# Performance work log

Hardware: AMD Instinct MI355X
Metric: run time of the kernel (lower is better)

## Reference

```python
import jax, jax.numpy as jnp
import numpy as np

# Module hyperparameters (match torch init_kwargs)
D_MODEL = 512
N_HEADS = 8
WINDOW_LEN = 128
DIL_FACTOR = 64
N_DIL = 2
ATTN_SINK = True
SRC_LEN = 2048
BSZ = 2


def setup_inputs() -> dict:
    key = jax.random.key(0)
    ks = jax.random.split(key, 6)
    w_scale = 0.04  # ~ xavier_uniform scale for 512x512
    inp = {
        "x": jax.random.normal(ks[0], (SRC_LEN, BSZ, D_MODEL), jnp.float32),
        "Wq": jax.random.normal(ks[1], (D_MODEL, D_MODEL), jnp.float32) * w_scale,
        "bq": jnp.zeros((D_MODEL,), jnp.float32),
        "Wk": jax.random.normal(ks[2], (D_MODEL, D_MODEL), jnp.float32) * w_scale,
        "bk": jnp.zeros((D_MODEL,), jnp.float32),
        "Wv": jax.random.normal(ks[3], (D_MODEL, D_MODEL), jnp.float32) * w_scale,
        "bv": jnp.zeros((D_MODEL,), jnp.float32),
        "Wo": jax.random.normal(ks[4], (D_MODEL, D_MODEL), jnp.float32) * w_scale,
        "bo": jnp.zeros((D_MODEL,), jnp.float32),
        "beta": jnp.zeros((N_HEADS,), jnp.float32),
    }
    return inp


def _fast_attention(x, Wq, bq, Wk, bk, Wv, bv, Wo, bo, beta):
    s, b, dm = x.shape  # (src_len, bsz, d_model)
    h = N_HEADS
    d = dm // h
    q = x @ Wq.T + bq
    k = x @ Wk.T + bk
    v = x @ Wv.T + bv

    def split_heads(t):  # 's b (h d) -> (b h) s d'
        return t.reshape(s, b, h, d).transpose(1, 2, 0, 3).reshape(b * h, s, d)

    q, k, v = split_heads(q), split_heads(k), split_heads(v)

    # beta: per-head temperature, tiled over batch (matches torch .repeat(bsz,1,1))
    beta_e = jnp.tile(jnp.exp(beta), b)[:, None, None]  # (b*h, 1, 1)
    q = q / (jnp.sqrt(jnp.asarray(d, q.dtype)) * beta_e)

    attn_out = jnp.zeros_like(v)
    z = b * h
    for i in range(N_DIL):
        dil = DIL_FACTOR ** i
        p = (WINDOW_LEN - 1) * dil
        pad = (p % s) if (p % s) != p else 0  # static python ints
        nw = pad // dil + 1  # num windows
        # causal left-padded strided windowed view of q: (z, nw, s, d)
        qp = jnp.pad(q, ((0, 0), (pad, 0), (0, 0)))
        idx = (jnp.arange(nw) * dil)[:, None] + jnp.arange(s)[None, :]  # (nw, s)
        qi = qp[:, idx, :]
        w = jnp.einsum('zbsd,zsd->zbs', qi, k)  # (z, nw, s)
        if ATTN_SINK:
            w = jnp.concatenate([w, jnp.zeros((z, 1, s), w.dtype)], axis=1)
        w = jax.nn.softmax(w, axis=1)  # softmax over window axis (+ sink)
        if ATTN_SINK:
            w = w[:, :-1]
        k2 = jnp.einsum('zbs,zsd->zbd', w, k)  # (z, nw, d)
        v2 = jnp.einsum('zbs,zsd->zbd', w, v)
        # left-pad back to full length (zeros at front, values at end)
        k = jnp.pad(k2, ((0, 0), (s - nw, 0), (0, 0)))
        v = jnp.pad(v2, ((0, 0), (s - nw, 0), (0, 0)))
        attn_out = attn_out + v

    # '(b h) s d -> s b (h d)'
    out = attn_out.reshape(b, h, s, d).transpose(2, 0, 1, 3).reshape(s, b, dm)
    return out @ Wo.T + bo


def reference(x, Wq, bq, Wk, bk, Wv, bv, Wo, bo, beta):
    return _fast_attention(x, Wq, bq, Wk, bk, Wv, bv, Wo, bo, beta)
```

## Files before the change

kernel.cpp:

```cpp
#include <hip/hip_runtime.h>
#include <hip/hip_bf16.h>
#include <math.h>

#define S_LEN 2048
#define BSZ 2
#define DM 512
#define NH 8
#define HD 64
#define RTOT (S_LEN*BSZ)
#define T_KEEP 32
#define ROW0 ((S_LEN - T_KEEP)*BSZ)
#define NXELEM (RTOT*DM)
#define NWROW  (NH*128)
#define NWELEM (NWROW*DM)

typedef __attribute__((ext_vector_type(8))) _Float16 half8;
typedef __attribute__((ext_vector_type(4))) float floatx4;

__device__ __forceinline__ void gld16(const void* g, void* l) {
    __builtin_amdgcn_global_load_lds((const __attribute__((address_space(1))) void*)g,
                                     (__attribute__((address_space(3))) void*)l, 16, 0, 0);
}

__device__ __forceinline__ short cvt1(float v) {
    _Float16 h = (_Float16)v;
    return __builtin_bit_cast(short, h);
}

__global__ __launch_bounds__(256) void convert(
    const float* __restrict__ x,
    const float* __restrict__ Wq, const float* __restrict__ Wk,
    const float* __restrict__ bq, const float* __restrict__ bk,
    const float* __restrict__ bo,
    short* __restrict__ xf, short* __restrict__ wf, float* __restrict__ bcat,
    float* __restrict__ sig, float* __restrict__ sbar, float* __restrict__ Ssum,
    float* __restrict__ out)
{
    const int g = blockIdx.x*blockDim.x + threadIdx.x;
    const int stride = gridDim.x*blockDim.x;
    const int total4 = (NXELEM + NWELEM)/4;
    for (int i = g; i < total4; i += stride) {
        float4 v; size_t dst; short* d;
        if (i < NXELEM/4) {
            v = ((const float4*)x)[i];
            dst = (size_t)i*4; d = xf;
        } else {
            int e = (i - NXELEM/4)*4;
            int R = e >> 9;
            int k = e & 511;
            int h = R >> 7;
            int p = R & 127;
            int m = p >> 6;
            int c = p & 63;
            const float* W = m ? Wk : Wq;
            v = *(const float4*)&W[(size_t)(h*HD + c)*DM + k];
            dst = (size_t)R*DM + k; d = wf;
        }
        short4 hv;
        hv.x = cvt1(v.x); hv.y = cvt1(v.y); hv.z = cvt1(v.z); hv.w = cvt1(v.w);
        *(short4*)&d[dst] = hv;
    }
    {
        const float4* b4 = (const float4*)bo;
        float4* o4 = (float4*)out;
        const int fill4 = ROW0*DM/4;
        for (int i = g; i < fill4; i += stride) o4[i] = b4[i & 127];
    }
    if (g < NWROW) {
        int h = g >> 7, p = g & 127, m = p >> 6, c = p & 63;
        bcat[g] = (m ? bk : bq)[h*HD + c];
    }
    if (g < NH*RTOT) sig[g] = 0.f;
    if (g < 16*DM)   sbar[g] = 0.f;
    if (g < 16)      Ssum[g] = 0.f;
}

__global__ __launch_bounds__(256, 2) void qk_gemm(
    const _Float16* __restrict__ xf, const _Float16* __restrict__ wf,
    const float* __restrict__ bcat,
    float* __restrict__ sig, float* __restrict__ qsel)
{
    __shared__ __align__(16) char smem[65536];

    const int tid  = threadIdx.x;
    const int w    = tid >> 6;
    const int lane = tid & 63;
    const int lrow = lane & 15;
    const int lk8  = lane >> 4;
    const int rc   = blockIdx.x;
    const int h    = blockIdx.y;
    const int jh   = blockIdx.z;
    const int r0   = rc * 128;

    {
        const int t = w;
        const int bcol = (t < 2) ? (jh*32 + t*16) : (64 + jh*32 + (t-2)*16);
        const _Float16* src = wf + (size_t)(h*128 + bcol + lrow)*DM + lk8*8;
        for (int ci = 0; ci < 16; ++ci)
            gld16(src + ci*32, smem + (w*16 + ci)*1024);
    }
    __syncthreads();

    const float bq0 = bcat[h*128 + jh*32 + lrow];
    const float bq1 = bcat[h*128 + jh*32 + 16 + lrow];
    const float bk0 = bcat[h*128 + 64 + jh*32 + lrow];
    const float bk1 = bcat[h*128 + 64 + jh*32 + 16 + lrow];

    #pragma unroll
    for (int nn = 0; nn < 2; ++nn) {
        const int n = w + nn*4;
        const int rbase = r0 + n*16;

        half8 A[16];
        const _Float16* pa = xf + (size_t)(rbase + lrow)*DM + lk8*8;
        #pragma unroll
        for (int kc = 0; kc < 16; ++kc)
            A[kc] = *(const half8*)(pa + kc*32);

        floatx4 aq0 = (floatx4)0.f, aq1 = (floatx4)0.f;
        floatx4 ak0 = (floatx4)0.f, ak1 = (floatx4)0.f;
        #pragma unroll
        for (int kc = 0; kc < 16; ++kc) {
            half8 b0 = *(const half8*)(smem + ( 0 + kc)*1024 + lane*16);
            half8 b1 = *(const half8*)(smem + (16 + kc)*1024 + lane*16);
            half8 b2 = *(const half8*)(smem + (32 + kc)*1024 + lane*16);
            half8 b3 = *(const half8*)(smem + (48 + kc)*1024 + lane*16);
            aq0 = __builtin_amdgcn_mfma_f32_16x16x32_f16(A[kc], b0, aq0, 0, 0, 0);
            aq1 = __builtin_amdgcn_mfma_f32_16x16x32_f16(A[kc], b1, aq1, 0, 0, 0);
            ak0 = __builtin_amdgcn_mfma_f32_16x16x32_f16(A[kc], b2, ak0, 0, 0, 0);
            ak1 = __builtin_amdgcn_mfma_f32_16x16x32_f16(A[kc], b3, ak1, 0, 0, 0);
        }

        #pragma unroll
        for (int r = 0; r < 4; ++r) {
            float q0 = aq0[r] + bq0, q1 = aq1[r] + bq1;
            float k0 = ak0[r] + bk0, k1 = ak1[r] + bk1;
            float p = q0*k0 + q1*k1;
            p += __shfl_xor(p, 1, 64);
            p += __shfl_xor(p, 2, 64);
            p += __shfl_xor(p, 4, 64);
            p += __shfl_xor(p, 8, 64);
            int row = rbase + lk8*4 + r;
            if (lrow == 0) atomicAdd(&sig[h*RTOT + row], p);
            if (((row >> 1) & 63) == 63) {
                int b  = row & 1;
                int wi = row >> 7;
                float* qd = &qsel[((size_t)(b*NH + h)*T_KEEP + wi)*64];
                qd[jh*32 + lrow]      = q0;
                qd[jh*32 + 16 + lrow] = q1;
            }
        }
    }
}

__global__ __launch_bounds__(256) void sbark(
    const float* __restrict__ x, const float* __restrict__ sigr,
    const float* __restrict__ beta, float* __restrict__ sbar,
    float* __restrict__ Ssum)
{
    __shared__ float ss[64][NH];
    const int tid = threadIdx.x;
    const int b = blockIdx.x & 1;
    const int s0 = (blockIdx.x >> 1) * 64;

    for (int i = tid; i < 64*NH; i += 256) {
        int s = i >> 3, hh = i & 7;
        float raw = sigr[hh*RTOT + (s0 + s)*2 + b];
        float isc = 1.0f / (8.0f * expf(beta[hh]));
        ss[s][hh] = 1.0f / (1.0f + expf(-raw * isc));
    }
    __syncthreads();
    if (tid < NH) {
        float t = 0.f;
        for (int s = 0; s < 64; ++s) t += ss[s][tid];
        atomicAdd(&Ssum[b*NH + tid], t);
    }
    #pragma unroll
    for (int cp = 0; cp < 2; ++cp) {
        int c = cp*256 + tid;
        float a8[NH];
        #pragma unroll
        for (int hh = 0; hh < NH; ++hh) a8[hh] = 0.f;
        for (int s = 0; s < 64; ++s) {
            float xv = x[(size_t)((s0 + s)*2 + b)*DM + c];
            #pragma unroll
            for (int hh = 0; hh < NH; ++hh) a8[hh] += ss[s][hh] * xv;
        }
        #pragma unroll
        for (int hh = 0; hh < NH; ++hh)
            atomicAdd(&sbar[(b*NH + hh)*DM + c], a8[hh]);
    }
}

__global__ __launch_bounds__(256) void headk(
    const float* __restrict__ qsel, const float* __restrict__ beta,
    const float* __restrict__ sbar, const float* __restrict__ Ssum,
    const float* __restrict__ Wk, const float* __restrict__ bk,
    const float* __restrict__ Wv, const float* __restrict__ bv,
    const float* __restrict__ Wo,
    float* __restrict__ coef, float* __restrict__ G)
{
    const int z = blockIdx.x;
    const int h = z & 7;
    const int tid = threadIdx.x;

    __shared__ float s_sb[DM];
    __shared__ float s_red[64][4];
    __shared__ float s_kb[64], s_vb[64];
    __shared__ float s_part[T_KEEP][8];
    __shared__ float s_gp[64][4];

    s_sb[tid]       = sbar[z*DM + tid];
    s_sb[tid + 256] = sbar[z*DM + 256 + tid];
    __syncthreads();
    const float S = Ssum[z];

    {
        int j = tid >> 2, kp = tid & 3;
        const float* wr = &Wk[(size_t)(h*HD + j)*DM + kp*128];
        float a = 0.f;
        #pragma unroll
        for (int k = 0; k < 128; k += 4) {
            float4 w4 = *(const float4*)&wr[k];
            int k0 = kp*128 + k;
            a += w4.x*s_sb[k0] + w4.y*s_sb[k0+1] + w4.z*s_sb[k0+2] + w4.w*s_sb[k0+3];
        }
        s_red[j][kp] = a;
    }
    __syncthreads();
    if (tid < 64) s_kb[tid] = s_red[tid][0]+s_red[tid][1]+s_red[tid][2]+s_red[tid][3]
                              + bk[h*HD + tid]*S;
    __syncthreads();
    {
        int j = tid >> 2, kp = tid & 3;
        const float* wr = &Wv[(size_t)(h*HD + j)*DM + kp*128];
        float a = 0.f;
        #pragma unroll
        for (int k = 0; k < 128; k += 4) {
            float4 w4 = *(const float4*)&wr[k];
            int k0 = kp*128 + k;
            a += w4.x*s_sb[k0] + w4.y*s_sb[k0+1] + w4.z*s_sb[k0+2] + w4.w*s_sb[k0+3];
        }
        s_red[j][kp] = a;
    }
    __syncthreads();
    if (tid < 64) s_vb[tid] = s_red[tid][0]+s_red[tid][1]+s_red[tid][2]+s_red[tid][3]
                              + bv[h*HD + tid]*S;
    __syncthreads();

    {
        int wi = tid >> 3, jg = tid & 7;
        const float* qrow = &qsel[((size_t)z*T_KEEP + wi)*64 + jg*8];
        float4 q1 = *(const float4*)qrow;
        float4 q2 = *(const float4*)(qrow + 4);
        int j0 = jg*8;
        float p = q1.x*s_kb[j0] + q1.y*s_kb[j0+1] + q1.z*s_kb[j0+2] + q1.w*s_kb[j0+3]
                + q2.x*s_kb[j0+4] + q2.y*s_kb[j0+5] + q2.z*s_kb[j0+6] + q2.w*s_kb[j0+7];
        s_part[wi][jg] = p;
    }
    __syncthreads();
    if (tid < T_KEEP) {
        float sc = 0.f;
        #pragma unroll
        for (int gg = 0; gg < 8; ++gg) sc += s_part[tid][gg];
        sc *= 1.0f / (8.0f * expf(beta[h]));
        float m = sc;
        #pragma unroll
        for (int off = 16; off > 0; off >>= 1) m = fmaxf(m, __shfl_xor(m, off, 64));
        m = fmaxf(m, 0.f);
        float e = expf(sc - m);
        float d = e;
        #pragma unroll
        for (int off = 16; off > 0; off >>= 1) d += __shfl_xor(d, off, 64);
        d += expf(-m);
        float c = e / d;
        if (tid == T_KEEP-1) c += 1.0f;
        coef[z*T_KEEP + tid] = c;
    }

    const int cq = tid >> 2;
    const int jg = tid & 3;
    #pragma unroll
    for (int it = 0; it < 8; ++it) {
        int c = it*64 + cq;
        const float* wrow = &Wo[(size_t)c*DM + h*HD + jg*16];
        float a = 0.f;
        #pragma unroll
        for (int jj = 0; jj < 16; jj += 4) {
            float4 wv = *(const float4*)&wrow[jj];
            int j0 = jg*16 + jj;
            a += wv.x*s_vb[j0] + wv.y*s_vb[j0+1] + wv.z*s_vb[j0+2] + wv.w*s_vb[j0+3];
        }
        s_gp[cq][jg] = a;
        __syncthreads();
        if (tid < 64)
            G[(size_t)z*DM + it*64 + tid] = s_gp[tid][0] + s_gp[tid][1] + s_gp[tid][2] + s_gp[tid][3];
        __syncthreads();
    }
}

__global__ __launch_bounds__(256) void outk3(
    const float* __restrict__ coef, const float* __restrict__ G,
    const float* __restrict__ bo, float* __restrict__ out)
{
    const int a = blockIdx.x;
    const int b = a & 1;
    const int wi = a >> 1;
    const int tid = threadIdx.x;
    __shared__ float s_cf[NH];
    if (tid < NH) s_cf[tid] = coef[(b*NH + tid)*T_KEEP + wi];
    __syncthreads();
    for (int c = tid; c < DM; c += 256) {
        float v = bo[c];
        #pragma unroll
        for (int h = 0; h < NH; ++h)
            v += s_cf[h] * G[(size_t)(b*NH + h)*DM + c];
        out[(size_t)(ROW0 + a)*DM + c] = v;
    }
}

extern "C" void kernel_launch(void* const* d_in, const int* in_sizes, int n_in,
                              void* d_out, int out_size, void* d_ws, size_t ws_size,
                              hipStream_t stream) {
    const float* x    = (const float*)d_in[0];
    const float* Wq   = (const float*)d_in[1];
    const float* bq   = (const float*)d_in[2];
    const float* Wk   = (const float*)d_in[3];
    const float* bk   = (const float*)d_in[4];
    const float* Wv   = (const float*)d_in[5];
    const float* bv   = (const float*)d_in[6];
    const float* Wo   = (const float*)d_in[7];
    const float* bo   = (const float*)d_in[8];
    const float* beta = (const float*)d_in[9];

    char* ws = (char*)d_ws;
    float* sig  = (float*)(ws + 0);
    float* qsel = (float*)(ws + 131072);
    float* sbar = (float*)(ws + 262144);
    float* Ssum = (float*)(ws + 294912);
    float* bcat = (float*)(ws + 295168);
    float* coef = (float*)(ws + 299264);
    float* G    = (float*)(ws + 301312);
    short* xf   = (short*)(ws + 335872);
    short* wf   = (short*)(ws + 335872 + 4194304);
    float* out  = (float*)d_out;

    convert<<<2048, 256, 0, stream>>>(x, Wq, Wk, bq, bk, bo,
                                      xf, wf, bcat, sig, sbar, Ssum, out);
    dim3 g1(32, NH, 2);
    qk_gemm<<<g1, 256, 0, stream>>>((const _Float16*)xf, (const _Float16*)wf,
                                    bcat, sig, qsel);
    sbark<<<64, 256, 0, stream>>>(x, sig, beta, sbar, Ssum);
    headk<<<16, 256, 0, stream>>>(qsel, beta, sbar, Ssum, Wk, bk, Wv, bv, Wo, coef, G);
    outk3<<<64, 256, 0, stream>>>(coef, G, bo, out);
}
```

Measured before the change: 126.2 us.

## Fuse sigmoid/sbar reduction into QK GEMM and restructure head/output kernels

The QK GEMM now has each block compute all 128 Q/K columns for a head and double-buffer the weight tiles in swizzled LDS. It applies the sigmoid and the weighted x reduction in-kernel, which removes the global sig buffer, its atomics and the separate sbark kernel. The head kernel is split so the K and V projections run on separate blocks. The Wo projection and output writes are merged into one kernel parallelised over output columns. This cuts the launch count and serial per-head work, at the cost of higher register pressure (occupancy 1) and more atomics into sbar.

Measured after the change: 113.4 us. 10.1% less time.

```diff
diff --git a/kernel.cpp b/kernel.cpp
--- a/kernel.cpp
+++ b/kernel.cpp
@@ -1,5 +1,4 @@
 #include <hip/hip_runtime.h>
-#include <hip/hip_bf16.h>
 #include <math.h>
 
 #define S_LEN 2048
@@ -30,10 +29,9 @@
 __global__ __launch_bounds__(256) void convert(
     const float* __restrict__ x,
     const float* __restrict__ Wq, const float* __restrict__ Wk,
-    const float* __restrict__ bq, const float* __restrict__ bk,
     const float* __restrict__ bo,
-    short* __restrict__ xf, short* __restrict__ wf, float* __restrict__ bcat,
-    float* __restrict__ sig, float* __restrict__ sbar, float* __restrict__ Ssum,
+    short* __restrict__ xf, short* __restrict__ wf,
+    float* __restrict__ sbar, float* __restrict__ Ssum,
     float* __restrict__ out)
 {
     const int g = blockIdx.x*blockDim.x + threadIdx.x;
@@ -66,19 +64,17 @@
         const int fill4 = ROW0*DM/4;
         for (int i = g; i < fill4; i += stride) o4[i] = b4[i & 127];
     }
-    if (g < NWROW) {
-        int h = g >> 7, p = g & 127, m = p >> 6, c = p & 63;
-        bcat[g] = (m ? bk : bq)[h*HD + c];
-    }
-    if (g < NH*RTOT) sig[g] = 0.f;
-    if (g < 16*DM)   sbar[g] = 0.f;
-    if (g < 16)      Ssum[g] = 0.f;
-}
-
-__global__ __launch_bounds__(256, 2) void qk_gemm(
+    if (g < 16*DM) sbar[g] = 0.f;
+    if (g < 16)    Ssum[g] = 0.f;
+}
+
+__global__ __launch_bounds__(256, 1) void qk_sig(
     const _Float16* __restrict__ xf, const _Float16* __restrict__ wf,
-    const float* __restrict__ bcat,
-    float* __restrict__ sig, float* __restrict__ qsel)
+    const float* __restrict__ x,
+    const float* __restrict__ bq, const float* __restrict__ bk,
+    const float* __restrict__ beta,
+    float* __restrict__ sbar, float* __restrict__ Ssum,
+    float* __restrict__ qsel)
 {
     __shared__ __align__(16) char smem[65536];
 
@@ -87,137 +83,153 @@
     const int lane = tid & 63;
     const int lrow = lane & 15;
     const int lk8  = lane >> 4;
-    const int rc   = blockIdx.x;
-    const int h    = blockIdx.y;
-    const int jh   = blockIdx.z;
+    const int bid  = blockIdx.x;
+    const int rc   = (bid & 7)*4 + (bid >> 6);
+    const int h    = (bid >> 3) & 7;
     const int r0   = rc * 128;
 
-    {
-        const int t = w;
-        const int bcol = (t < 2) ? (jh*32 + t*16) : (64 + jh*32 + (t-2)*16);
-        const _Float16* src = wf + (size_t)(h*128 + bcol + lrow)*DM + lk8*8;
-        for (int ci = 0; ci < 16; ++ci)
-            gld16(src + ci*32, smem + (w*16 + ci)*1024);
-    }
-    __syncthreads();
-
-    const float bq0 = bcat[h*128 + jh*32 + lrow];
-    const float bq1 = bcat[h*128 + jh*32 + 16 + lrow];
-    const float bk0 = bcat[h*128 + 64 + jh*32 + lrow];
-    const float bk1 = bcat[h*128 + 64 + jh*32 + 16 + lrow];
-
-    #pragma unroll
-    for (int nn = 0; nn < 2; ++nn) {
-        const int n = w + nn*4;
-        const int rbase = r0 + n*16;
-
-        half8 A[16];
-        const _Float16* pa = xf + (size_t)(rbase + lrow)*DM + lk8*8;
-        #pragma unroll
-        for (int kc = 0; kc < 16; ++kc)
-            A[kc] = *(const half8*)(pa + kc*32);
-
-        floatx4 aq0 = (floatx4)0.f, aq1 = (floatx4)0.f;
-        floatx4 ak0 = (floatx4)0.f, ak1 = (floatx4)0.f;
-        #pragma unroll
-        for (int kc = 0; kc < 16; ++kc) {
-            half8 b0 = *(const half8*)(smem + ( 0 + kc)*1024 + lane*16);
-            half8 b1 = *(const half8*)(smem + (16 + kc)*1024 + lane*16);
-            half8 b2 = *(const half8*)(smem + (32 + kc)*1024 + lane*16);
-            half8 b3 = *(const half8*)(smem + (48 + kc)*1024 + lane*16);
-            aq0 = __builtin_amdgcn_mfma_f32_16x16x32_f16(A[kc], b0, aq0, 0, 0, 0);
-            aq1 = __builtin_amdgcn_mfma_f32_16x16x32_f16(A[kc], b1, aq1, 0, 0, 0);
-            ak0 = __builtin_amdgcn_mfma_f32_16x16x32_f16(A[kc], b2, ak0, 0, 0, 0);
-            ak1 = __builtin_amdgcn_mfma_f32_16x16x32_f16(A[kc], b3, ak1, 0, 0, 0);
-        }
-
+    const int jsub  = lk8;
+    const int sslot = lrow ^ (jsub << 2);
+    const _Float16* wsrc = wf + (size_t)(h*128 + w*32 + jsub)*DM + sslot*8;
+
+    #pragma unroll
+    for (int i = 0; i < 8; ++i)
+        gld16(wsrc + (size_t)(4*i)*DM, smem + (w*8 + i)*1024);
+
+    const int rbA = r0 + w*16;
+    const int rbB = r0 + (w+4)*16;
+    const _Float16* paA = xf + (size_t)(rbA + lrow)*DM + lk8*8;
+    const _Float16* paB = xf + (size_t)(rbB + lrow)*DM + lk8*8;
+
+    floatx4 acc[2][8];
+    #pragma unroll
+    for (int jt = 0; jt < 8; ++jt) { acc[0][jt] = (floatx4)0.f; acc[1][jt] = (floatx4)0.f; }
+
+    half8 Aa[2][4], Ab[2][4];
+    #pragma unroll
+    for (int kc2 = 0; kc2 < 4; ++kc2) {
+        Aa[0][kc2] = *(const half8*)(paA + kc2*32);
+        Ab[0][kc2] = *(const half8*)(paB + kc2*32);
+    }
+
+    __syncthreads();
+
+    #pragma unroll
+    for (int kq = 0; kq < 4; ++kq) {
+        const int cur = kq & 1, nxt = cur ^ 1;
+        if (kq < 3) {
+            #pragma unroll
+            for (int kc2 = 0; kc2 < 4; ++kc2) {
+                Aa[nxt][kc2] = *(const half8*)(paA + ((kq+1)*4 + kc2)*32);
+                Ab[nxt][kc2] = *(const half8*)(paB + ((kq+1)*4 + kc2)*32);
+            }
+            char* nb = smem + nxt*32768;
+            #pragma unroll
+            for (int i = 0; i < 8; ++i)
+                gld16(wsrc + (size_t)(4*i)*DM + (kq+1)*128, nb + (w*8 + i)*1024);
+        }
+        const char* buf = smem + cur*32768;
+        #pragma unroll
+        for (int kc2 = 0; kc2 < 4; ++kc2) {
+            #pragma unroll
+            for (int jt = 0; jt < 8; ++jt) {
+                const int j = jt*16 + lrow;
+                const int slotp = (kc2*4 + lk8) ^ ((lrow & 3) << 2);
+                half8 bf = *(const half8*)(buf + j*256 + slotp*16);
+                acc[0][jt] = __builtin_amdgcn_mfma_f32_16x16x32_f16(Aa[cur][kc2], bf, acc[0][jt], 0, 0, 0);
+                acc[1][jt] = __builtin_amdgcn_mfma_f32_16x16x32_f16(Ab[cur][kc2], bf, acc[1][jt], 0, 0, 0);
+            }
+        }
+        __syncthreads();
+    }
+
+    float* s_sig = (float*)smem;
+    float bqv[4], bkv[4];
+    #pragma unroll
+    for (int jt = 0; jt < 4; ++jt) {
+        bqv[jt] = bq[h*HD + jt*16 + lrow];
+        bkv[jt] = bk[h*HD + jt*16 + lrow];
+    }
+    const float isc = 1.0f / (8.0f * expf(beta[h]));
+
+    #pragma unroll
+    for (int t = 0; t < 2; ++t) {
         #pragma unroll
         for (int r = 0; r < 4; ++r) {
-            float q0 = aq0[r] + bq0, q1 = aq1[r] + bq1;
-            float k0 = ak0[r] + bk0, k1 = ak1[r] + bk1;
-            float p = q0*k0 + q1*k1;
+            float q[4]; float p = 0.f;
+            #pragma unroll
+            for (int jt = 0; jt < 4; ++jt) {
+                float qv = acc[t][jt][r]   + bqv[jt];
+                float kv = acc[t][jt+4][r] + bkv[jt];
+                q[jt] = qv;
+                p += qv * kv;
+            }
             p += __shfl_xor(p, 1, 64);
             p += __shfl_xor(p, 2, 64);
             p += __shfl_xor(p, 4, 64);
             p += __shfl_xor(p, 8, 64);
-            int row = rbase + lk8*4 + r;
-            if (lrow == 0) atomicAdd(&sig[h*RTOT + row], p);
-            if (((row >> 1) & 63) == 63) {
-                int b  = row & 1;
-                int wi = row >> 7;
-                float* qd = &qsel[((size_t)(b*NH + h)*T_KEEP + wi)*64];
-                qd[jh*32 + lrow]      = q0;
-                qd[jh*32 + 16 + lrow] = q1;
+            const int rowl = (w + t*4)*16 + lk8*4 + r;
+            if (lrow == 0)
+                s_sig[rowl] = 1.0f / (1.0f + expf(-p * isc));
+            if (rowl >= 126) {
+                const int b = rowl & 1;
+                float* qd = &qsel[((size_t)((b*NH + h)*T_KEEP) + rc)*64];
+                #pragma unroll
+                for (int jt = 0; jt < 4; ++jt) qd[jt*16 + lrow] = q[jt];
             }
         }
     }
-}
-
-__global__ __launch_bounds__(256) void sbark(
-    const float* __restrict__ x, const float* __restrict__ sigr,
-    const float* __restrict__ beta, float* __restrict__ sbar,
-    float* __restrict__ Ssum)
-{
-    __shared__ float ss[64][NH];
-    const int tid = threadIdx.x;
-    const int b = blockIdx.x & 1;
-    const int s0 = (blockIdx.x >> 1) * 64;
-
-    for (int i = tid; i < 64*NH; i += 256) {
-        int s = i >> 3, hh = i & 7;
-        float raw = sigr[hh*RTOT + (s0 + s)*2 + b];
-        float isc = 1.0f / (8.0f * expf(beta[hh]));
-        ss[s][hh] = 1.0f / (1.0f + expf(-raw * isc));
-    }
-    __syncthreads();
-    if (tid < NH) {
-        float t = 0.f;
-        for (int s = 0; s < 64; ++s) t += ss[s][tid];
-        atomicAdd(&Ssum[b*NH + tid], t);
-    }
-    #pragma unroll
-    for (int cp = 0; cp < 2; ++cp) {
-        int c = cp*256 + tid;
-        float a8[NH];
-        #pragma unroll
-        for (int hh = 0; hh < NH; ++hh) a8[hh] = 0.f;
-        for (int s = 0; s < 64; ++s) {
-            float xv = x[(size_t)((s0 + s)*2 + b)*DM + c];
-            #pragma unroll
-            for (int hh = 0; hh < NH; ++hh) a8[hh] += ss[s][hh] * xv;
-        }
-        #pragma unroll
-        for (int hh = 0; hh < NH; ++hh)
-            atomicAdd(&sbar[(b*NH + hh)*DM + c], a8[hh]);
-    }
-}
-
-__global__ __launch_bounds__(256) void headk(
-    const float* __restrict__ qsel, const float* __restrict__ beta,
+    __syncthreads();
+
+    {
+        const int b  = tid & 1;
+        const int cg = tid >> 1;
+        const float* px = x + (size_t)(r0 + b)*DM + cg*4;
+        float a0=0.f, a1=0.f, a2=0.f, a3=0.f;
+        #pragma unroll 8
+        for (int si = 0; si < 64; ++si) {
+            const float sg = s_sig[si*2 + b];
+            const float4 xv = *(const float4*)(px + (size_t)(si*2)*DM);
+            a0 += sg*xv.x; a1 += sg*xv.y; a2 += sg*xv.z; a3 += sg*xv.w;
+        }
+        float* sd = &sbar[(size_t)(b*NH + h)*DM + cg*4];
+        atomicAdd(sd+0, a0); atomicAdd(sd+1, a1);
+        atomicAdd(sd+2, a2); atomicAdd(sd+3, a3);
+    }
+    if (tid < 2) {
+        float s = 0.f;
+        for (int i = 0; i < 64; ++i) s += s_sig[i*2 + tid];
+        atomicAdd(&Ssum[tid*NH + h], s);
+    }
+}
+
+__global__ __launch_bounds__(256) void kvbar_coef(
     const float* __restrict__ sbar, const float* __restrict__ Ssum,
     const float* __restrict__ Wk, const float* __restrict__ bk,
     const float* __restrict__ Wv, const float* __restrict__ bv,
-    const float* __restrict__ Wo,
-    float* __restrict__ coef, float* __restrict__ G)
+    const float* __restrict__ qsel, const float* __restrict__ beta,
+    float* __restrict__ vbar, float* __restrict__ coef)
 {
-    const int z = blockIdx.x;
-    const int h = z & 7;
+    const int z  = blockIdx.x >> 1;
+    const int kv = blockIdx.x & 1;
+    const int h  = z & 7;
     const int tid = threadIdx.x;
 
     __shared__ float s_sb[DM];
     __shared__ float s_red[64][4];
-    __shared__ float s_kb[64], s_vb[64];
+    __shared__ float s_kb[64];
     __shared__ float s_part[T_KEEP][8];
-    __shared__ float s_gp[64][4];
 
     s_sb[tid]       = sbar[z*DM + tid];
     s_sb[tid + 256] = sbar[z*DM + 256 + tid];
     __syncthreads();
     const float S = Ssum[z];
 
-    {
-        int j = tid >> 2, kp = tid & 3;
-        const float* wr = &Wk[(size_t)(h*HD + j)*DM + kp*128];
+    const float* W    = kv ? Wv : Wk;
+    const float* bvec = kv ? bv : bk;
+    {
+        const int j = tid >> 2, kp = tid & 3;
+        const float* wr = &W[(size_t)(h*HD + j)*DM + kp*128];
         float a = 0.f;
         #pragma unroll
         for (int k = 0; k < 128; k += 4) {
@@ -228,33 +240,21 @@
         s_red[j][kp] = a;
     }
     __syncthreads();
-    if (tid < 64) s_kb[tid] = s_red[tid][0]+s_red[tid][1]+s_red[tid][2]+s_red[tid][3]
-                              + bk[h*HD + tid]*S;
-    __syncthreads();
-    {
-        int j = tid >> 2, kp = tid & 3;
-        const float* wr = &Wv[(size_t)(h*HD + j)*DM + kp*128];
-        float a = 0.f;
-        #pragma unroll
-        for (int k = 0; k < 128; k += 4) {
-            float4 w4 = *(const float4*)&wr[k];
-            int k0 = kp*128 + k;
-            a += w4.x*s_sb[k0] + w4.y*s_sb[k0+1] + w4.z*s_sb[k0+2] + w4.w*s_sb[k0+3];
-        }
-        s_red[j][kp] = a;
-    }
-    __syncthreads();
-    if (tid < 64) s_vb[tid] = s_red[tid][0]+s_red[tid][1]+s_red[tid][2]+s_red[tid][3]
-                              + bv[h*HD + tid]*S;
-    __syncthreads();
-
-    {
-        int wi = tid >> 3, jg = tid & 7;
+    if (tid < 64) {
+        float val = s_red[tid][0]+s_red[tid][1]+s_red[tid][2]+s_red[tid][3]
+                  + bvec[h*HD + tid]*S;
+        if (kv) vbar[z*HD + tid] = val;
+        else    s_kb[tid] = val;
+    }
+    if (kv) return;
+    __syncthreads();
+    {
+        const int wi = tid >> 3, jg = tid & 7;
         const float* qrow = &qsel[((size_t)z*T_KEEP + wi)*64 + jg*8];
         float4 q1 = *(const float4*)qrow;
         float4 q2 = *(const float4*)(qrow + 4);
-        int j0 = jg*8;
-        float p = q1.x*s_kb[j0] + q1.y*s_kb[j0+1] + q1.z*s_kb[j0+2] + q1.w*s_kb[j0+3]
+        const int j0 = jg*8;
+        float p = q1.x*s_kb[j0]   + q1.y*s_kb[j0+1] + q1.z*s_kb[j0+2] + q1.w*s_kb[j0+3]
                 + q2.x*s_kb[j0+4] + q2.y*s_kb[j0+5] + q2.z*s_kb[j0+6] + q2.w*s_kb[j0+7];
         s_part[wi][jg] = p;
     }
@@ -277,45 +277,51 @@
         if (tid == T_KEEP-1) c += 1.0f;
         coef[z*T_KEEP + tid] = c;
     }
-
-    const int cq = tid >> 2;
-    const int jg = tid & 3;
-    #pragma unroll
-    for (int it = 0; it < 8; ++it) {
-        int c = it*64 + cq;
-        const float* wrow = &Wo[(size_t)c*DM + h*HD + jg*16];
+}
+
+__global__ __launch_bounds__(256) void gout(
+    const float* __restrict__ coef, const float* __restrict__ vbar,
+    const float* __restrict__ Wo, const float* __restrict__ bo,
+    float* __restrict__ out)
+{
+    const int b  = blockIdx.x & 1;
+    const int cc = blockIdx.x >> 1;
+    const int tid = threadIdx.x;
+
+    __shared__ float s_cf[NH][T_KEEP];
+    __shared__ float s_vb[NH*HD];
+    __shared__ float s_gp[16][NH][2];
+
+    s_vb[tid]       = vbar[b*512 + tid];
+    s_vb[tid + 256] = vbar[b*512 + 256 + tid];
+    s_cf[tid >> 5][tid & 31] = coef[((size_t)(b*NH) + (tid >> 5))*T_KEEP + (tid & 31)];
+    __syncthreads();
+
+    {
+        const int ci = tid & 15, hh = (tid >> 4) & 7, j2 = tid >> 7;
+        const float* wr = &Wo[(size_t)(cc*16 + ci)*DM + hh*HD + j2*32];
+        const float* vb = &s_vb[hh*HD + j2*32];
         float a = 0.f;
         #pragma unroll
-        for (int jj = 0; jj < 16; jj += 4) {
-            float4 wv = *(const float4*)&wrow[jj];
-            int j0 = jg*16 + jj;
-            a += wv.x*s_vb[j0] + wv.y*s_vb[j0+1] + wv.z*s_vb[j0+2] + wv.w*s_vb[j0+3];
-        }
-        s_gp[cq][jg] = a;
-        __syncthreads();
-        if (tid < 64)
-            G[(size_t)z*DM + it*64 + tid] = s_gp[tid][0] + s_gp[tid][1] + s_gp[tid][2] + s_gp[tid][3];
-        __syncthreads();
-    }
-}
-
-__global__ __launch_bounds__(256) void outk3(
-    const float* __restrict__ coef, const float* __restrict__ G,
-    const float* __restrict__ bo, float* __restrict__ out)
-{
-    const int a = blockIdx.x;
-    const int b = a & 1;
-    const int wi = a >> 1;
-    const int tid = threadIdx.x;
-    __shared__ float s_cf[NH];
-    if (tid < NH) s_cf[tid] = coef[(b*NH + tid)*T_KEEP + wi];
-    __syncthreads();
-    for (int c = tid; c < DM; c += 256) {
-        float v = bo[c];
-        #pragma unroll
-        for (int h = 0; h < NH; ++h)
-            v += s_cf[h] * G[(size_t)(b*NH + h)*DM + c];
-        out[(size_t)(ROW0 + a)*DM + c] = v;
+        for (int j = 0; j < 32; j += 4) {
+            float4 w4 = *(const float4*)&wr[j];
+            a += w4.x*vb[j] + w4.y*vb[j+1] + w4.z*vb[j+2] + w4.w*vb[j+3];
+        }
+        s_gp[ci][hh][j2] = a;
+    }
+    __syncthreads();
+    {
+        const int ci = tid & 15;
+        const float bov = bo[cc*16 + ci];
+        #pragma unroll
+        for (int hf = 0; hf < 2; ++hf) {
+            const int wi = (tid >> 4) + hf*16;
+            float v = bov;
+            #pragma unroll
+            for (int hh = 0; hh < NH; ++hh)
+                v += s_cf[hh][wi] * (s_gp[ci][hh][0] + s_gp[ci][hh][1]);
+            out[(size_t)(ROW0 + wi*2 + b)*DM + cc*16 + ci] = v;
+        }
     }
 }
 
@@ -334,23 +340,18 @@
     const float* beta = (const float*)d_in[9];
 
     char* ws = (char*)d_ws;
-    float* sig  = (float*)(ws + 0);
-    float* qsel = (float*)(ws + 131072);
-    float* sbar = (float*)(ws + 262144);
-    float* Ssum = (float*)(ws + 294912);
-    float* bcat = (float*)(ws + 295168);
-    float* coef = (float*)(ws + 299264);
-    float* G    = (float*)(ws + 301312);
-    short* xf   = (short*)(ws + 335872);
-    short* wf   = (short*)(ws + 335872 + 4194304);
+    float* qsel = (float*)(ws + 0);
+    float* sbar = (float*)(ws + 131072);
+    float* Ssum = (float*)(ws + 163840);
+    float* coef = (float*)(ws + 164096);
+    float* vbar = (float*)(ws + 166144);
+    short* xf   = (short*)(ws + 262144);
+    short* wf   = (short*)(ws + 262144 + 4194304);
     float* out  = (float*)d_out;
 
-    convert<<<2048, 256, 0, stream>>>(x, Wq, Wk, bq, bk, bo,
-                                      xf, wf, bcat, sig, sbar, Ssum, out);
-    dim3 g1(32, NH, 2);
-    qk_gemm<<<g1, 256, 0, stream>>>((const _Float16*)xf, (const _Float16*)wf,
-                                    bcat, sig, qsel);
-    sbark<<<64, 256, 0, stream>>>(x, sig, beta, sbar, Ssum);
-    headk<<<16, 256, 0, stream>>>(qsel, beta, sbar, Ssum, Wk, bk, Wv, bv, Wo, coef, G);
-    outk3<<<64, 256, 0, stream>>>(coef, G, bo, out);
-}
+    convert<<<2048, 256, 0, stream>>>(x, Wq, Wk, bo, xf, wf, sbar, Ssum, out);
+    qk_sig<<<256, 256, 0, stream>>>((const _Float16*)xf, (const _Float16*)wf, x,
+                                    bq, bk, beta, sbar, Ssum, qsel);
+    kvbar_coef<<<32, 256, 0, stream>>>(sbar, Ssum, Wk, bk, Wv, bv, qsel, beta, vbar, coef);
+    gout<<<64, 256, 0, stream>>>(coef, vbar, Wo, bo, out);
+}
```
